# Optimization experiments

Measured on AMD Instinct MI355X. Metric: run time of the kernel, lower is better.

## Reference

```python
import jax, jax.numpy as jnp
import numpy as np

EPS = 1e-6

def setup_inputs() -> dict:
    key = jax.random.key(0)
    ks = jax.random.split(key, 8)
    I, S, O = 1024, 512, 1024
    Bsz, T = 4, 2048
    return {
        "u": jax.random.normal(ks[0], (Bsz, T, I), dtype=jnp.float32),
        "dt": jax.random.normal(ks[1], (S,), dtype=jnp.float32),
        "A": jax.random.normal(ks[2], (S,), dtype=jnp.float32),
        "Bmat": jax.random.normal(ks[3], (I, S), dtype=jnp.float32) / np.sqrt(S),
        "C": jax.random.normal(ks[4], (S, O), dtype=jnp.float32) / np.sqrt(S),
        "D": jax.random.normal(ks[5], (O,), dtype=jnp.float32),
        "norm_w": jnp.ones((I,), dtype=jnp.float32),
    }

def _rmsnorm(x, w):
    x32 = x.astype(jnp.float32)
    n = x32 * jax.lax.rsqrt(jnp.mean(x32 * x32, axis=-1, keepdims=True) + EPS)
    return n.astype(x.dtype) * w

def reference(u, dt, A, Bmat, C, D, norm_w):
    u = _rmsnorm(u, norm_w)                      # [B, T, I]
    Bsz, T, _ = u.shape
    dts = jax.nn.sigmoid(dt)                     # [S]
    a = jnp.exp(-dts * jnp.abs(A))               # [S] discretized decay
    t = jnp.arange(T, dtype=jnp.float32)
    h = dts[:, None] * a[:, None] ** t[None, :]  # [S, T] geometric kernel
    u_proj = jnp.einsum('bti,is->bst', u, Bmat)  # [B, S, T]
    # depthwise causal conv: flipped kernel + cross-correlation == convolution
    k = jnp.flip(h, axis=1)[:, None, :]          # [S, 1, T] (OIW)
    x = jax.lax.conv_general_dilated(
        u_proj, k, window_strides=(1,), padding=[(T - 1, T - 1)],
        dimension_numbers=('NCW', 'OIW', 'NCW'),
        feature_group_count=u_proj.shape[1])[:, :, :T]  # [B, S, T]
    x = jnp.transpose(x, (0, 2, 1))              # [B, T, S]
    y = jnp.einsum('bts,so->bto', x, C) + D      # [B, T, O]
    return (y, x[:, -1])
```

## Files before the change

### kernel.cpp

```cpp
#include <hip/hip_runtime.h>
#include <math.h>

#define I_DIM 1024
#define S_DIM 512
#define O_DIM 1024
#define T_DIM 2048
#define B_SZ 4
#define M_ROWS (B_SZ * T_DIM)
#define EPSF 1e-6f

#define CL 64
#define NCH 32

typedef _Float16 f16;
typedef __attribute__((ext_vector_type(8))) _Float16 f16x8;
typedef __attribute__((ext_vector_type(2))) _Float16 f16x2;
typedef __attribute__((ext_vector_type(4))) float f32x4;

__device__ __forceinline__ unsigned short f2h_bits(float f) {
    _Float16 h = (_Float16)f;
    return __builtin_bit_cast(unsigned short, h);
}

__device__ __forceinline__ void load16_lds(const void* g, void* l) {
    __builtin_amdgcn_global_load_lds((const __attribute__((address_space(1))) void*)g,
                                     (__attribute__((address_space(3))) void*)l,
                                     16, 0, 0);
}

__global__ __launch_bounds__(256)
void prep_w(const float* __restrict__ Bmat, const float* __restrict__ dt,
            const float* __restrict__ nw, unsigned short* __restrict__ Bt16,
            const float* __restrict__ Cmat, unsigned short* __restrict__ Ct16) {
    __shared__ float tile[32][33];
    const int t = threadIdx.x;
    const int tx = t & 31, ty = t >> 5;
    const int bx = blockIdx.x;
    if (bx < 512) {
        const int bs = (bx & 15) * 32;
        const int bi = (bx >> 4) * 32;
        #pragma unroll
        for (int i = ty; i < 32; i += 8)
            tile[i][tx] = Bmat[(size_t)(bi + i) * S_DIM + bs + tx];
        __syncthreads();
        const float w = nw[bi + tx];
        #pragma unroll
        for (int i = ty; i < 32; i += 8) {
            const int s = bs + i;
            const float dts = 1.0f / (1.0f + expf(-dt[s]));
            Bt16[(size_t)s * I_DIM + bi + tx] = f2h_bits(tile[tx][i] * dts * w);
        }
    } else {
        const int tb = bx - 512;
        const int bo = (tb & 31) * 32;
        const int bs = (tb >> 5) * 32;
        #pragma unroll
        for (int i = ty; i < 32; i += 8)
            tile[i][tx] = Cmat[(size_t)(bs + i) * O_DIM + bo + tx];
        __syncthreads();
        #pragma unroll
        for (int i = ty; i < 32; i += 8)
            Ct16[(size_t)(bo + i) * S_DIM + bs + tx] = f2h_bits(tile[tx][i]);
    }
}

__global__ __launch_bounds__(256)
void gemm1_rms_chfin(const float* __restrict__ U, const f16* __restrict__ Bt,
                     f16* __restrict__ up, float* __restrict__ chlast,
                     const float* __restrict__ dt, const float* __restrict__ Avec) {
    constexpr int K = I_DIM, N = S_DIM, LDA = 80, NK = K / 32;
    __shared__ __align__(16) unsigned char AsB[2][64 * LDA];
    __shared__ f16 Bs[2][128 * 32];
    __shared__ float rsbuf[64];
    const int t = threadIdx.x;

    int bid = blockIdx.x;
    bid = (bid & 7) * 64 + (bid >> 3);
    const int n0 = (bid & 3) * 128;
    const int m0 = (bid >> 2) * 64;
    const int wid = t >> 6, lane = t & 63;
    const int wn = wid * 32, lr = lane & 15, kg = lane >> 4;

    const float* aptr = U + (size_t)(m0 + (t >> 2)) * K + (t & 3) * 8;
    const int bswz = ((t & 3) ^ ((t >> 3) & 3)) * 8;
    const f16* bptr = Bt + (size_t)(n0 + (t >> 2)) * K + bswz;
    unsigned char* adst0 = &AsB[0][(t >> 2) * LDA + (t & 3) * 16];
    unsigned char* adst1 = &AsB[1][(t >> 2) * LDA + (t & 3) * 16];
    const int bread = (kg ^ ((lr >> 1) & 3)) * 8;

    float ss = 0.f;
    f32x4 acc[4][2];
    #pragma unroll
    for (int i = 0; i < 4; ++i)
        #pragma unroll
        for (int j = 0; j < 2; ++j) acc[i][j] = (f32x4){0.f, 0.f, 0.f, 0.f};

    float4 ra, rb;
    auto cvt_write = [&](unsigned char* dst) {
        ss += ra.x * ra.x + ra.y * ra.y + ra.z * ra.z + ra.w * ra.w
            + rb.x * rb.x + rb.y * rb.y + rb.z * rb.z + rb.w * rb.w;
        f16x8 h = { (_Float16)ra.x, (_Float16)ra.y, (_Float16)ra.z, (_Float16)ra.w,
                    (_Float16)rb.x, (_Float16)rb.y, (_Float16)rb.z, (_Float16)rb.w };
        *(f16x8*)dst = h;
    };

    load16_lds(bptr, &Bs[0][t * 8]);
    load16_lds(bptr + (size_t)64 * K, &Bs[0][2048 + t * 8]);
    ra = *(const float4*)(aptr);
    rb = *(const float4*)(aptr + 4);
    cvt_write(adst0);
    asm volatile("s_waitcnt vmcnt(0) lgkmcnt(0)");
    __builtin_amdgcn_s_barrier();

    for (int kt = 0; kt < NK; ++kt) {
        const int cur = kt & 1;
        if (kt + 1 < NK) {
            const int k1 = (kt + 1) * 32;
            ra = *(const float4*)(aptr + k1);
            rb = *(const float4*)(aptr + k1 + 4);
            load16_lds(bptr + k1, &Bs[cur ^ 1][t * 8]);
            load16_lds(bptr + (size_t)64 * K + k1, &Bs[cur ^ 1][2048 + t * 8]);
            asm volatile("s_waitcnt vmcnt(4)");
        } else {
            asm volatile("s_waitcnt vmcnt(0)");
        }
        __builtin_amdgcn_s_barrier();
        __builtin_amdgcn_sched_barrier(0);

        f16x8 af[4], bf[2];
        #pragma unroll
        for (int m = 0; m < 4; ++m)
            af[m] = *(const f16x8*)&AsB[cur][(m * 16 + lr) * LDA + kg * 16];
        #pragma unroll
        for (int n = 0; n < 2; ++n)
            bf[n] = *(const f16x8*)&Bs[cur][(wn + n * 16 + lr) * 32 + bread];
        #pragma unroll
        for (int m = 0; m < 4; ++m)
            #pragma unroll
            for (int n = 0; n < 2; ++n)
                acc[m][n] = __builtin_amdgcn_mfma_f32_16x16x32_f16(af[m], bf[n], acc[m][n], 0, 0, 0);

        if (kt + 1 < NK)
            cvt_write(cur == 0 ? adst1 : adst0);
        asm volatile("s_waitcnt lgkmcnt(0)");
        __builtin_amdgcn_sched_barrier(0);
        __builtin_amdgcn_s_barrier();
    }

    ss += __shfl_xor(ss, 1, 64);
    ss += __shfl_xor(ss, 2, 64);
    if ((t & 3) == 0) rsbuf[t >> 2] = rsqrtf(ss * (1.0f / K) + EPSF);
    __syncthreads();

    const int cb = m0 >> 11;
    const int cc = (m0 >> 6) & (NCH - 1);
    #pragma unroll
    for (int n = 0; n < 2; ++n) {
        const int col = n0 + wn + n * 16 + lr;
        const float dts = 1.0f / (1.0f + expf(-dt[col]));
        const float e = dts * fabsf(Avec[col]);
        const float ainv = expf(e);
        float partial = 0.f;
        #pragma unroll
        for (int m = 0; m < 4; ++m) {
            const int row = m * 16 + kg * 4;
            f32x4 rs4 = *(const f32x4*)&rsbuf[row];
            float wgt = expf(-e * (float)(63 - row));
            #pragma unroll
            for (int j = 0; j < 4; ++j) {
                const float val = rs4[j] * acc[m][n][j];
                up[(size_t)(m0 + row + j) * N + col] = (_Float16)val;
                partial = fmaf(wgt, val, partial);
                wgt *= ainv;
            }
        }
        partial += __shfl_xor(partial, 16, 64);
        partial += __shfl_xor(partial, 32, 64);
        if (kg == 0)
            chlast[(size_t)(cb * NCH + cc) * S_DIM + col] = partial;
    }
}

__global__ __launch_bounds__(256)
void gemm2_scan(const f16* __restrict__ upb, const float* __restrict__ chlast,
                const f16* __restrict__ Ct, const float* __restrict__ Dvec,
                const float* __restrict__ dt, const float* __restrict__ Avec,
                float* __restrict__ y, float* __restrict__ xlast) {
    constexpr int K = S_DIM, N = O_DIM, NK = K / 32;
    __shared__ __align__(16) unsigned char As[64 * 1024];
    __shared__ f16 Bs[2][128 * 32];
    const int t = threadIdx.x;

    int bid = blockIdx.x;
    bid = (bid & 7) * 128 + (bid >> 3);
    const int n0 = (bid & 7) * 128;
    const int m0 = (bid >> 3) * 64;
    const int wid = t >> 6, lane = t & 63;
    const int wn = wid * 32, lr = lane & 15, kg = lane >> 4;

    const int bswz = ((t & 3) ^ ((t >> 3) & 3)) * 8;
    const f16* bptr = Ct + (size_t)(n0 + (t >> 2)) * K + bswz;
    load16_lds(bptr, &Bs[0][t * 8]);
    load16_lds(bptr + (size_t)64 * K, &Bs[0][2048 + t * 8]);
    const int bread = (kg ^ ((lr >> 1) & 3)) * 8;

    const int cc = (m0 >> 6) & (NCH - 1);
    const int cb = m0 >> 11;
    const int s0 = 2 * t;
    const float dts0 = 1.0f / (1.0f + expf(-dt[s0]));
    const float dts1 = 1.0f / (1.0f + expf(-dt[s0 + 1]));
    const float ab0 = fabsf(Avec[s0]), ab1 = fabsf(Avec[s0 + 1]);
    const float g0 = expf(-dts0 * ab0);
    const float g1 = expf(-dts1 * ab1);
    const float gCL0 = expf(-dts0 * ab0 * (float)CL);
    const float gCL1 = expf(-dts1 * ab1 * (float)CL);
    const float2* ch = (const float2*)chlast;
    float cy0 = 0.f, cy1 = 0.f;
    for (int j = 0; j < cc; ++j) {
        float2 f = ch[(size_t)(cb * NCH + j) * 256 + t];
        cy0 = fmaf(gCL0, cy0, f.x);
        cy1 = fmaf(gCL1, cy1, f.y);
    }

    const unsigned* up32 = (const unsigned*)upb;
    const size_t ub = (size_t)m0 * 256 + t;
    unsigned v[CL];
    #pragma unroll
    for (int j = 0; j < CL; ++j) v[j] = up32[ub + (size_t)j * 256];
    float x0 = cy0, x1 = cy1;
    #pragma unroll
    for (int j = 0; j < CL; ++j) {
        f16x2 h = __builtin_bit_cast(f16x2, v[j]);
        x0 = fmaf(g0, x0, (float)h.x);
        x1 = fmaf(g1, x1, (float)h.y);
        f16x2 o; o.x = (_Float16)x0; o.y = (_Float16)x1;
        v[j] = __builtin_bit_cast(unsigned, o);
    }
    #pragma unroll
    for (int j = 0; j < CL; ++j)
        *(unsigned*)&As[j * 1024 + ((t * 4) ^ ((j & 7) << 4))] = v[j];
    if (cc == NCH - 1)
        ((float2*)xlast)[cb * 256 + t] = make_float2(x0, x1);
    __syncthreads();

    f32x4 acc[4][2];
    #pragma unroll
    for (int i = 0; i < 4; ++i)
        #pragma unroll
        for (int j = 0; j < 2; ++j) acc[i][j] = (f32x4){0.f, 0.f, 0.f, 0.f};

    const int swz = (lr & 7) << 4;
    for (int kt = 0; kt < NK; ++kt) {
        const int cur = kt & 1;
        if (kt + 1 < NK) {
            const int k1 = (kt + 1) * 32;
            load16_lds(bptr + k1, &Bs[cur ^ 1][t * 8]);
            load16_lds(bptr + (size_t)64 * K + k1, &Bs[cur ^ 1][2048 + t * 8]);
            asm volatile("s_waitcnt vmcnt(2)");
        } else {
            asm volatile("s_waitcnt vmcnt(0)");
        }
        __builtin_amdgcn_s_barrier();
        __builtin_amdgcn_sched_barrier(0);

        f16x8 af[4], bf[2];
        #pragma unroll
        for (int m = 0; m < 4; ++m)
            af[m] = *(const f16x8*)&As[(m * 16 + lr) * 1024 + ((kt * 64 + kg * 16) ^ swz)];
        #pragma unroll
        for (int n = 0; n < 2; ++n)
            bf[n] = *(const f16x8*)&Bs[cur][(wn + n * 16 + lr) * 32 + bread];
        #pragma unroll
        for (int m = 0; m < 4; ++m)
            #pragma unroll
            for (int n = 0; n < 2; ++n)
                acc[m][n] = __builtin_amdgcn_mfma_f32_16x16x32_f16(af[m], bf[n], acc[m][n], 0, 0, 0);
        __builtin_amdgcn_s_barrier();
    }

    #pragma unroll
    for (int n = 0; n < 2; ++n) {
        const int col = n0 + wn + n * 16 + lr;
        const float dv = Dvec[col];
        #pragma unroll
        for (int m = 0; m < 4; ++m) {
            const int row = m0 + m * 16 + kg * 4;
            #pragma unroll
            for (int j = 0; j < 4; ++j)
                y[(size_t)(row + j) * N + col] = acc[m][n][j] + dv;
        }
    }
}

extern "C" void kernel_launch(void* const* d_in, const int* in_sizes, int n_in,
                              void* d_out, int out_size, void* d_ws, size_t ws_size,
                              hipStream_t stream) {
    const float* u    = (const float*)d_in[0];
    const float* dt   = (const float*)d_in[1];
    const float* Avec = (const float*)d_in[2];
    const float* Bmat = (const float*)d_in[3];
    const float* Cmat = (const float*)d_in[4];
    const float* Dvec = (const float*)d_in[5];
    const float* nw   = (const float*)d_in[6];

    float* y     = (float*)d_out;
    float* xlast = y + (size_t)M_ROWS * O_DIM;

    char* w = (char*)d_ws;
    f16*            up16   = (f16*)(w);
    unsigned short* Bt16   = (unsigned short*)(w + 8388608);
    unsigned short* Ct16   = (unsigned short*)(w + 9437184);
    float*          chlast = (float*)(w + 10485760);

    prep_w<<<1024, 256, 0, stream>>>(Bmat, dt, nw, Bt16, Cmat, Ct16);

    gemm1_rms_chfin<<<512, 256, 0, stream>>>(u, (const f16*)Bt16, up16, chlast, dt, Avec);

    gemm2_scan<<<1024, 256, 0, stream>>>(up16, chlast, (const f16*)Ct16, Dvec,
                                         dt, Avec, y, xlast);
}
```

Before: 66.48 us.

## Triple-buffer GEMM1 LDS with one barrier per k-step and unroll carry loop

GEMM1 moves from double-buffered A/B shared-memory tiles to a three-slot ring. Global A loads run two k-steps ahead in alternating register sets, and the fp16 conversion is written one step ahead, which drops the second barrier per iteration. The A tile now uses the same XOR-swizzled 32-wide layout as B instead of padded rows. Separately, gemm2's chunk-carry prefix loop is unrolled by four to issue more independent loads. The cost is more LDS and registers, which may lower occupancy.

```diff
diff --git a/kernel.cpp b/kernel.cpp
--- a/kernel.cpp
+++ b/kernel.cpp
@@ -68,9 +68,9 @@
 void gemm1_rms_chfin(const float* __restrict__ U, const f16* __restrict__ Bt,
                      f16* __restrict__ up, float* __restrict__ chlast,
                      const float* __restrict__ dt, const float* __restrict__ Avec) {
-    constexpr int K = I_DIM, N = S_DIM, LDA = 80, NK = K / 32;
-    __shared__ __align__(16) unsigned char AsB[2][64 * LDA];
-    __shared__ f16 Bs[2][128 * 32];
+    constexpr int K = I_DIM, N = S_DIM, NK = K / 32;
+    __shared__ f16 As[3][64 * 32];
+    __shared__ f16 Bs[3][128 * 32];
     __shared__ float rsbuf[64];
     const int t = threadIdx.x;
 
@@ -81,12 +81,11 @@
     const int wid = t >> 6, lane = t & 63;
     const int wn = wid * 32, lr = lane & 15, kg = lane >> 4;
 
-    const float* aptr = U + (size_t)(m0 + (t >> 2)) * K + (t & 3) * 8;
-    const int bswz = ((t & 3) ^ ((t >> 3) & 3)) * 8;
-    const f16* bptr = Bt + (size_t)(n0 + (t >> 2)) * K + bswz;
-    unsigned char* adst0 = &AsB[0][(t >> 2) * LDA + (t & 3) * 16];
-    unsigned char* adst1 = &AsB[1][(t >> 2) * LDA + (t & 3) * 16];
-    const int bread = (kg ^ ((lr >> 1) & 3)) * 8;
+    const int swch = (t & 3) ^ ((t >> 3) & 3);
+    const float* aptr = U + (size_t)(m0 + (t >> 2)) * K + swch * 8;
+    const f16*  bptr = Bt + (size_t)(n0 + (t >> 2)) * K + swch * 8;
+    const int rchunk = (kg ^ ((lr >> 1) & 3)) * 8;
+    f16* adst = (f16*)&As[0][0] + t * 8;
 
     float ss = 0.f;
     f32x4 acc[4][2];
@@ -95,56 +94,60 @@
         #pragma unroll
         for (int j = 0; j < 2; ++j) acc[i][j] = (f32x4){0.f, 0.f, 0.f, 0.f};
 
-    float4 ra, rb;
-    auto cvt_write = [&](unsigned char* dst) {
-        ss += ra.x * ra.x + ra.y * ra.y + ra.z * ra.z + ra.w * ra.w
-            + rb.x * rb.x + rb.y * rb.y + rb.z * rb.z + rb.w * rb.w;
-        f16x8 h = { (_Float16)ra.x, (_Float16)ra.y, (_Float16)ra.z, (_Float16)ra.w,
-                    (_Float16)rb.x, (_Float16)rb.y, (_Float16)rb.z, (_Float16)rb.w };
-        *(f16x8*)dst = h;
+    float4 rga[2], rgb[2];
+
+    auto stageB = [&](int kt, int slot) {
+        load16_lds(bptr + kt * 32, &Bs[slot][t * 8]);
+        load16_lds(bptr + (size_t)64 * K + kt * 32, &Bs[slot][2048 + t * 8]);
     };
-
-    load16_lds(bptr, &Bs[0][t * 8]);
-    load16_lds(bptr + (size_t)64 * K, &Bs[0][2048 + t * 8]);
-    ra = *(const float4*)(aptr);
-    rb = *(const float4*)(aptr + 4);
-    cvt_write(adst0);
-    asm volatile("s_waitcnt vmcnt(0) lgkmcnt(0)");
-    __builtin_amdgcn_s_barrier();
-
+    auto writeA = [&](const float4* r, int slot) {
+        ss += r[0].x * r[0].x + r[0].y * r[0].y + r[0].z * r[0].z + r[0].w * r[0].w
+            + r[1].x * r[1].x + r[1].y * r[1].y + r[1].z * r[1].z + r[1].w * r[1].w;
+        f16x8 h = { (_Float16)r[0].x, (_Float16)r[0].y, (_Float16)r[0].z, (_Float16)r[0].w,
+                    (_Float16)r[1].x, (_Float16)r[1].y, (_Float16)r[1].z, (_Float16)r[1].w };
+        *(f16x8*)(adst + slot * 2048) = h;
+    };
+
+    rga[0] = *(const float4*)(aptr);
+    rga[1] = *(const float4*)(aptr + 4);
+    stageB(0, 0);
+    rgb[0] = *(const float4*)(aptr + 32);
+    rgb[1] = *(const float4*)(aptr + 36);
+    stageB(1, 1);
+    asm volatile("s_waitcnt vmcnt(6)");
+    writeA(rga, 0);
+
+    #pragma unroll 2
     for (int kt = 0; kt < NK; ++kt) {
-        const int cur = kt & 1;
-        if (kt + 1 < NK) {
-            const int k1 = (kt + 1) * 32;
-            ra = *(const float4*)(aptr + k1);
-            rb = *(const float4*)(aptr + k1 + 4);
-            load16_lds(bptr + k1, &Bs[cur ^ 1][t * 8]);
-            load16_lds(bptr + (size_t)64 * K + k1, &Bs[cur ^ 1][2048 + t * 8]);
-            asm volatile("s_waitcnt vmcnt(4)");
-        } else {
-            asm volatile("s_waitcnt vmcnt(0)");
-        }
+        asm volatile("s_waitcnt lgkmcnt(0)");
+        if (kt + 1 < NK) asm volatile("s_waitcnt vmcnt(2)");
+        else             asm volatile("s_waitcnt vmcnt(0)");
         __builtin_amdgcn_s_barrier();
         __builtin_amdgcn_sched_barrier(0);
 
+        if (kt + 1 < NK)
+            writeA(((kt + 1) & 1) ? rgb : rga, (kt + 1) % 3);
+        if (kt + 2 < NK) {
+            float4* r = (kt & 1) ? rgb : rga;
+            const int k2 = (kt + 2) * 32;
+            r[0] = *(const float4*)(aptr + k2);
+            r[1] = *(const float4*)(aptr + k2 + 4);
+            stageB(kt + 2, (kt + 2) % 3);
+        }
+
+        const int slot = kt % 3;
         f16x8 af[4], bf[2];
         #pragma unroll
         for (int m = 0; m < 4; ++m)
-            af[m] = *(const f16x8*)&AsB[cur][(m * 16 + lr) * LDA + kg * 16];
+            af[m] = *(const f16x8*)&As[slot][(m * 16 + lr) * 32 + rchunk];
         #pragma unroll
         for (int n = 0; n < 2; ++n)
-            bf[n] = *(const f16x8*)&Bs[cur][(wn + n * 16 + lr) * 32 + bread];
+            bf[n] = *(const f16x8*)&Bs[slot][(wn + n * 16 + lr) * 32 + rchunk];
         #pragma unroll
         for (int m = 0; m < 4; ++m)
             #pragma unroll
             for (int n = 0; n < 2; ++n)
                 acc[m][n] = __builtin_amdgcn_mfma_f32_16x16x32_f16(af[m], bf[n], acc[m][n], 0, 0, 0);
-
-        if (kt + 1 < NK)
-            cvt_write(cur == 0 ? adst1 : adst0);
-        asm volatile("s_waitcnt lgkmcnt(0)");
-        __builtin_amdgcn_sched_barrier(0);
-        __builtin_amdgcn_s_barrier();
     }
 
     ss += __shfl_xor(ss, 1, 64);
@@ -198,11 +201,11 @@
     const int wid = t >> 6, lane = t & 63;
     const int wn = wid * 32, lr = lane & 15, kg = lane >> 4;
 
-    const int bswz = ((t & 3) ^ ((t >> 3) & 3)) * 8;
-    const f16* bptr = Ct + (size_t)(n0 + (t >> 2)) * K + bswz;
+    const int srcswz = ((t & 3) ^ ((t >> 3) & 3)) * 8;
+    const f16* bptr = Ct + (size_t)(n0 + (t >> 2)) * K + srcswz;
     load16_lds(bptr, &Bs[0][t * 8]);
     load16_lds(bptr + (size_t)64 * K, &Bs[0][2048 + t * 8]);
-    const int bread = (kg ^ ((lr >> 1) & 3)) * 8;
+    const int rchunk = (kg ^ ((lr >> 1) & 3)) * 8;
 
     const int cc = (m0 >> 6) & (NCH - 1);
     const int cb = m0 >> 11;
@@ -216,10 +219,23 @@
     const float gCL1 = expf(-dts1 * ab1 * (float)CL);
     const float2* ch = (const float2*)chlast;
     float cy0 = 0.f, cy1 = 0.f;
-    for (int j = 0; j < cc; ++j) {
-        float2 f = ch[(size_t)(cb * NCH + j) * 256 + t];
-        cy0 = fmaf(gCL0, cy0, f.x);
-        cy1 = fmaf(gCL1, cy1, f.y);
+    {
+        int j = 0;
+        for (; j + 4 <= cc; j += 4) {
+            float2 f0 = ch[(size_t)(cb * NCH + j + 0) * 256 + t];
+            float2 f1 = ch[(size_t)(cb * NCH + j + 1) * 256 + t];
+            float2 f2 = ch[(size_t)(cb * NCH + j + 2) * 256 + t];
+            float2 f3 = ch[(size_t)(cb * NCH + j + 3) * 256 + t];
+            cy0 = fmaf(gCL0, cy0, f0.x); cy1 = fmaf(gCL1, cy1, f0.y);
+            cy0 = fmaf(gCL0, cy0, f1.x); cy1 = fmaf(gCL1, cy1, f1.y);
+            cy0 = fmaf(gCL0, cy0, f2.x); cy1 = fmaf(gCL1, cy1, f2.y);
+            cy0 = fmaf(gCL0, cy0, f3.x); cy1 = fmaf(gCL1, cy1, f3.y);
+        }
+        for (; j < cc; ++j) {
+            float2 f = ch[(size_t)(cb * NCH + j) * 256 + t];
+            cy0 = fmaf(gCL0, cy0, f.x);
+            cy1 = fmaf(gCL1, cy1, f.y);
+        }
     }
 
     const unsigned* up32 = (const unsigned*)upb;
@@ -269,7 +285,7 @@
             af[m] = *(const f16x8*)&As[(m * 16 + lr) * 1024 + ((kt * 64 + kg * 16) ^ swz)];
         #pragma unroll
         for (int n = 0; n < 2; ++n)
-            bf[n] = *(const f16x8*)&Bs[cur][(wn + n * 16 + lr) * 32 + bread];
+            bf[n] = *(const f16x8*)&Bs[cur][(wn + n * 16 + lr) * 32 + rchunk];
         #pragma unroll
         for (int m = 0; m < 4; ++m)
             #pragma unroll
```

New measurement: 56.49 us. 1.18x faster.
